# Optimization experiments

Hardware: AMD Instinct MI355X
Metric: run time of the kernel (lower is better)

## Reference

```python
import jax, jax.numpy as jnp
import numpy as np

SHIFT_SIZE = 5
PAD = 2  # shift_size // 2
EPS = 1e-5


def layernorm(x, g, b):
    m = x.mean(-1, keepdims=True)
    v = ((x - m) ** 2).mean(-1, keepdims=True)
    return (x - m) / jnp.sqrt(v + EPS) * g + b


def axial_shift(x, H, W, D, axis):
    # x: (B, N, C) -> torch-style shift along spatial `axis` of (B,C,H,W,D)
    B, N, C = x.shape
    xn = x.transpose(0, 2, 1).reshape(B, C, H, W, D)
    xn = jnp.pad(xn, ((0, 0), (0, 0), (PAD, PAD), (PAD, PAD), (PAD, PAD)))
    cs = -(-C // SHIFT_SIZE)  # torch.chunk uses ceil-sized chunks
    rolled = [
        jnp.roll(xn[:, i * cs:min((i + 1) * cs, C)], s, axis=axis)
        for i, s in enumerate(range(-PAD, PAD + 1))
    ]
    xc = jnp.concatenate(rolled, axis=1)
    xc = xc[:, :, PAD:PAD + H, PAD:PAD + W, PAD:PAD + D]
    return xc.reshape(B, C, H * W * D).transpose(0, 2, 1)


def dwconv3d(x, w, b, H, W, D):
    # x: (B,N,C), w: (C,1,3,3,3) depthwise
    B, N, C = x.shape
    v = x.transpose(0, 2, 1).reshape(B, C, H, W, D)
    y = jax.lax.conv_general_dilated(
        v, w, window_strides=(1, 1, 1), padding=[(1, 1)] * 3,
        dimension_numbers=('NCDHW', 'OIDHW', 'NCDHW'), feature_group_count=C)
    y = y + b[None, :, None, None, None]
    return y.reshape(B, C, N).transpose(0, 2, 1)


def setup_inputs() -> dict:
    key = jax.random.key(0)
    ks = jax.random.split(key, 12)
    C_in, C = 4, 128
    x = jax.random.normal(ks[0], (1, C_in, 96, 96, 96), dtype=jnp.float32)
    p = {
        'x': x,
        'proj_w': jax.random.normal(ks[1], (C, C_in, 3, 3, 3), jnp.float32) * 0.05,
        'proj_b': jnp.zeros((C,), jnp.float32),
        'g0': jnp.ones((C,), jnp.float32), 'b0': jnp.zeros((C,), jnp.float32),
        'g2': jnp.ones((C,), jnp.float32), 'b2': jnp.zeros((C,), jnp.float32),
        'fc1_w': jax.random.normal(ks[2], (C, C), jnp.float32) * 0.02,
        'fc1_b': jnp.zeros((C,), jnp.float32),
        'dw1_w': jax.random.normal(ks[3], (C, 1, 3, 3, 3), jnp.float32) * 0.1,
        'dw1_b': jnp.zeros((C,), jnp.float32),
        'fc2_w': jax.random.normal(ks[4], (C, C), jnp.float32) * 0.02,
        'fc2_b': jnp.zeros((C,), jnp.float32),
        'dw2_w': jax.random.normal(ks[5], (C, 1, 3, 3, 3), jnp.float32) * 0.1,
        'dw2_b': jnp.zeros((C,), jnp.float32),
        'fc3_w': jax.random.normal(ks[6], (C, C), jnp.float32) * 0.02,
        'fc3_b': jnp.zeros((C,), jnp.float32),
        'gn': jnp.ones((C,), jnp.float32), 'bn': jnp.zeros((C,), jnp.float32),
    }
    return p


def reference(x, proj_w, proj_b, g0, b0, g2, b2, fc1_w, fc1_b, dw1_w, dw1_b,
              fc2_w, fc2_b, dw2_w, dw2_b, fc3_w, fc3_b, gn, bn):
    B = x.shape[0]
    # OverlapPatchEmbed: Conv3d(k=3, s=2, p=1)
    v = jax.lax.conv_general_dilated(
        x, proj_w, window_strides=(2, 2, 2), padding=[(1, 1)] * 3,
        dimension_numbers=('NCDHW', 'OIDHW', 'NCDHW'))
    v = v + proj_b[None, :, None, None, None]
    _, C, H, W, D = v.shape
    t = v.reshape(B, C, H * W * D).transpose(0, 2, 1)  # (B,N,C)
    t = layernorm(t, g0, b0)

    # unext_shifted_Block (dropout/droppath in eval -> identity)
    h = layernorm(t, g2, b2)
    h = axial_shift(h, H, W, D, axis=2)
    h = h @ fc1_w.T + fc1_b
    h = dwconv3d(h, dw1_w, dw1_b, H, W, D)
    h = axial_shift(h, H, W, D, axis=3)
    h = h @ fc2_w.T + fc2_b
    h = dwconv3d(h, dw2_w, dw2_b, H, W, D)
    h = axial_shift(h, H, W, D, axis=4)
    h = h @ fc3_w.T + fc3_b
    h = jax.nn.gelu(h, approximate=False)
    t = t + h

    t = layernorm(t, gn, bn)
    out = t.reshape(B, H, W, D, C).transpose(0, 4, 1, 2, 3)
    return out
```

## Files before the change

kernel.cpp:

```cpp
#include <hip/hip_runtime.h>
#include <hip/hip_bf16.h>
#include <math.h>

#define NTOT 110592
#define SD 48
#define SWD 2304

typedef short s16x8 __attribute__((ext_vector_type(8)));
typedef unsigned short u16x8 __attribute__((ext_vector_type(8)));
typedef unsigned short u16x4 __attribute__((ext_vector_type(4)));
typedef float f32x4 __attribute__((ext_vector_type(4)));
typedef unsigned short u16;

__device__ __forceinline__ float bf2f(u16 u) {
    unsigned int x = ((unsigned int)u) << 16;
    float f; __builtin_memcpy(&f, &x, 4); return f;
}
__device__ __forceinline__ u16 f2bf(float f) {
    __hip_bfloat16 h = __float2bfloat16(f);
    u16 u; __builtin_memcpy(&u, &h, 2); return u;
}
__device__ __forceinline__ u16x8 zero8() {
    u16x8 z;
    #pragma unroll
    for (int j = 0; j < 8; ++j) z[j] = 0;
    return z;
}

__device__ __forceinline__ float gelu_f(float x) {
    float y = x * (0.7978845608f + 0.0356774081f * x * x);
    float e = exp2f(y * 2.885390082f);
    return x - x * __builtin_amdgcn_rcpf(e + 1.f);
}

__device__ __forceinline__ u16x8 ld_shift8(const u16* __restrict__ in, int n, int coord,
                                           int STR, int cbase) {
    int g = cbase / 26;
    int split = 26 * (g + 1) - cbase;
    int sh0 = g - 2;
    int cs0 = coord - sh0;
    u16x8 lo = zero8();
    if (cs0 >= 0 && cs0 < SD) lo = *(const u16x8*)&in[(size_t)(n - sh0 * STR) * 128 + cbase];
    if (split >= 8) return lo;
    u16x8 hi = zero8();
    int cs1 = cs0 - 1;
    if (cs1 >= 0 && cs1 < SD) hi = *(const u16x8*)&in[(size_t)(n - (sh0 + 1) * STR) * 128 + cbase];
    u16x8 r;
    #pragma unroll
    for (int j = 0; j < 8; ++j) r[j] = (j < split) ? lo[j] : hi[j];
    return r;
}

__device__ __forceinline__ int dec_tap(int tau) {
    int ti = (tau >= 18 ? 1 : 0) + (tau >= 9 ? 1 : 0);
    int rem = tau - ti * 9;
    int tj = (rem >= 6 ? 1 : 0) + (rem >= 3 ? 1 : 0);
    int tk = rem - tj * 3;
    return ti * 2080 + tj * 416 + tk * 4;
}

__global__ __launch_bounds__(256) void k_prep(
    const float* __restrict__ pw, const float* __restrict__ fc1w,
    const float* __restrict__ fc2w, const float* __restrict__ fc3w,
    const float* __restrict__ dw1w, const float* __restrict__ dw2w,
    u16* __restrict__ wfP, u16* __restrict__ wf1, u16* __restrict__ wf2,
    u16* __restrict__ wf3, float* __restrict__ dwT1, float* __restrict__ dwT2)
{
    int b = blockIdx.x;
    if (b < 32) {
        int which = b >> 3;
        const float* src = (which == 0) ? pw : (which == 1) ? fc1w : (which == 2) ? fc2w : fc3w;
        u16* dst = (which == 0) ? wfP : (which == 1) ? wf1 : (which == 2) ? wf2 : wf3;
        int idx = (b & 7) * 256 + threadIdx.x;
        int lane = idx & 63;
        int s = (idx >> 6) & 3;
        int t = idx >> 8;
        int co = t * 16 + (lane & 15);
        int kb = s * 32 + (lane >> 4) * 8;
        #pragma unroll
        for (int j = 0; j < 8; ++j) {
            int kk = kb + j;
            float v;
            if (which == 0) {
                int tau = kk >> 2, ci = kk & 3;
                v = (tau < 27) ? src[co * 108 + ci * 27 + tau] : 0.f;
            } else {
                v = src[co * 128 + kk];
            }
            dst[idx * 8 + j] = f2bf(v);
        }
    } else {
        int which = (b - 32) / 14;
        int bb = (b - 32) % 14;
        const float* src = which ? dw2w : dw1w;
        float* dst = which ? dwT2 : dwT1;
        int idx = bb * 256 + threadIdx.x;
        if (idx < 27 * 128) {
            int k = idx >> 7;
            int co = idx & 127;
            dst[idx] = src[co * 27 + k];
        }
    }
}

__global__ __launch_bounds__(384) void k_proj_ln(
    const float* __restrict__ x, const u16* __restrict__ wfrag, const float* __restrict__ pb,
    const float* __restrict__ g0, const float* __restrict__ b0,
    const float* __restrict__ g2, const float* __restrict__ b2,
    u16* __restrict__ t_out, u16* __restrict__ h_out)
{
    __shared__ __align__(16) u16 sm[15 * 104 * 4];
    __shared__ __align__(16) u16 wfl[16384];
    const int tid = threadIdx.x;
    const int blk = blockIdx.x;
    const int n0 = blk * 96;
    const int oi = blk / 24;
    const int oj0 = (blk % 24) * 2;

    for (int i = tid; i < 2048; i += 384)
        *(u16x8*)&wfl[i * 8] = *(const u16x8*)&wfrag[i * 8];

    for (int pos = tid; pos < 15 * 98; pos += 384) {
        int r = pos / 98;
        int p = pos - r * 98;
        int ti = r / 5, sl = r - ti * 5;
        int iig = 2 * oi + ti - 1;
        int ijg = 2 * oj0 + sl - 1;
        int ik = p - 1;
        bool okv = (iig >= 0) && (iig < 96) && (ijg >= 0) && (ijg < 96) && (ik >= 0) && (ik < 96);
        u16x4 v;
        #pragma unroll
        for (int ci = 0; ci < 4; ++ci)
            v[ci] = okv ? f2bf(x[(((size_t)ci * 96 + iig) * 96 + ijg) * 96 + ik]) : (u16)0;
        *(u16x4*)&sm[(r * 104 + p) * 4] = v;
    }
    __syncthreads();

    const int lane = tid & 63;
    const int wv = tid >> 6;
    const int rb = wv * 16;
    const int colb = lane & 15;
    const int q = lane >> 4;
    const int arow = rb + colb;
    const int ojloc = (arow >= 48) ? 1 : 0;
    const int okk = arow - ojloc * 48;
    const int P = ojloc * 832 + okk * 8;

    int S[4][2];
    #pragma unroll
    for (int s = 0; s < 4; ++s) {
        int t0 = s * 8 + 2 * q;
        S[s][0] = dec_tap(t0);
        S[s][1] = dec_tap(t0 + 1);
    }

    f32x4 acc[8];
    #pragma unroll
    for (int t = 0; t < 8; ++t) {
        float bb = pb[t * 16 + colb];
        acc[t][0] = bb; acc[t][1] = bb; acc[t][2] = bb; acc[t][3] = bb;
    }
    #pragma unroll
    for (int s = 0; s < 4; ++s) {
        u16x4 v0 = *(const u16x4*)&sm[S[s][0] + P];
        u16x4 v1 = *(const u16x4*)&sm[S[s][1] + P];
        if (s == 3) {
            bool z0 = (q >= 2), z1 = (q >= 1);
            #pragma unroll
            for (int e = 0; e < 4; ++e) {
                if (z0) v0[e] = 0;
                if (z1) v1[e] = 0;
            }
        }
        s16x8 a;
        a[0] = (short)v0[0]; a[1] = (short)v0[1]; a[2] = (short)v0[2]; a[3] = (short)v0[3];
        a[4] = (short)v1[0]; a[5] = (short)v1[1]; a[6] = (short)v1[2]; a[7] = (short)v1[3];
        s16x8 bf[8];
        #pragma unroll
        for (int t = 0; t < 8; ++t)
            bf[t] = *(const s16x8*)&wfl[((t * 4 + s) * 64 + lane) * 8];
        #pragma unroll
        for (int t = 0; t < 8; ++t)
            acc[t] = __builtin_amdgcn_mfma_f32_16x16x32_bf16(a, bf[t], acc[t], 0, 0, 0);
    }

    float s1[4] = {0.f,0.f,0.f,0.f}, s2[4] = {0.f,0.f,0.f,0.f};
    #pragma unroll
    for (int t = 0; t < 8; ++t)
        #pragma unroll
        for (int r4 = 0; r4 < 4; ++r4) {
            float v = acc[t][r4];
            s1[r4] += v; s2[r4] += v * v;
        }
    #pragma unroll
    for (int r4 = 0; r4 < 4; ++r4)
        #pragma unroll
        for (int m = 1; m < 16; m <<= 1) {
            s1[r4] += __shfl_xor(s1[r4], m);
            s2[r4] += __shfl_xor(s2[r4], m);
        }

    float g0v[8], b0v[8], g2v[8], b2v[8];
    #pragma unroll
    for (int t = 0; t < 8; ++t) {
        int c = t * 16 + colb;
        g0v[t] = g0[c]; b0v[t] = b0[c]; g2v[t] = g2[c]; b2v[t] = b2[c];
    }

    float tval[8][4];
    float u1[4] = {0.f,0.f,0.f,0.f}, u2[4] = {0.f,0.f,0.f,0.f};
    #pragma unroll
    for (int r4 = 0; r4 < 4; ++r4) {
        float mean = s1[r4] * (1.f / 128.f);
        float var  = fmaxf(s2[r4] * (1.f / 128.f) - mean * mean, 0.f);
        float rstd = rsqrtf(var + 1e-5f);
        #pragma unroll
        for (int t = 0; t < 8; ++t) {
            float tv = (acc[t][r4] - mean) * rstd * g0v[t] + b0v[t];
            tval[t][r4] = tv;
            u1[r4] += tv; u2[r4] += tv * tv;
        }
    }
    #pragma unroll
    for (int r4 = 0; r4 < 4; ++r4) {
        #pragma unroll
        for (int m = 1; m < 16; m <<= 1) {
            u1[r4] += __shfl_xor(u1[r4], m);
            u2[r4] += __shfl_xor(u2[r4], m);
        }
    }

    #pragma unroll
    for (int r4 = 0; r4 < 4; ++r4) {
        float mean2 = u1[r4] * (1.f / 128.f);
        float var2  = fmaxf(u2[r4] * (1.f / 128.f) - mean2 * mean2, 0.f);
        float rstd2 = rsqrtf(var2 + 1e-5f);
        int row = rb + q * 4 + r4;
        size_t base = (size_t)(n0 + row) * 128;
        #pragma unroll
        for (int t = 0; t < 8; ++t) {
            int col = t * 16 + colb;
            float tv = tval[t][r4];
            t_out[base + col] = f2bf(tv);
            float hv = (tv - mean2) * rstd2 * g2v[t] + b2v[t];
            h_out[base + col] = f2bf(hv);
        }
    }
}

template <int AXIS>
__global__ __launch_bounds__(256) void k_shift_mm(
    const u16* __restrict__ in, const u16* __restrict__ wfrag, const float* __restrict__ bias,
    u16* __restrict__ out)
{
    __shared__ __align__(16) u16 wfl[16384];
    const int tid = threadIdx.x;
    const int n0 = blockIdx.x * 64;
    const int lane = tid & 63;
    const int wv = tid >> 6;
    const int colb = lane & 15;
    const int q = lane >> 4;

    for (int i = tid; i < 2048; i += 256)
        *(u16x8*)&wfl[i * 8] = *(const u16x8*)&wfrag[i * 8];

    const int arow = wv * 16 + colb;
    const int n = n0 + arow;
    const int STR = (AXIS == 0) ? SWD : (AXIS == 1) ? SD : 1;
    const int coord = (AXIS == 0) ? n / SWD : (AXIS == 1) ? (n / SD) % SD : n % SD;

    f32x4 acc[8];
    #pragma unroll
    for (int t = 0; t < 8; ++t) {
        float bb = bias[t * 16 + colb];
        acc[t][0] = bb; acc[t][1] = bb; acc[t][2] = bb; acc[t][3] = bb;
    }
    __syncthreads();
    #pragma unroll
    for (int s = 0; s < 4; ++s) {
        u16x8 av = ld_shift8(in, n, coord, STR, s * 32 + q * 8);
        s16x8 a = *(s16x8*)&av;
        s16x8 bf[8];
        #pragma unroll
        for (int t = 0; t < 8; ++t)
            bf[t] = *(const s16x8*)&wfl[((t * 4 + s) * 64 + lane) * 8];
        #pragma unroll
        for (int t = 0; t < 8; ++t)
            acc[t] = __builtin_amdgcn_mfma_f32_16x16x32_bf16(a, bf[t], acc[t], 0, 0, 0);
    }
    #pragma unroll
    for (int r4 = 0; r4 < 4; ++r4) {
        int row = wv * 16 + q * 4 + r4;
        size_t base = (size_t)(n0 + row) * 128;
        #pragma unroll
        for (int t = 0; t < 8; ++t)
            out[base + t * 16 + colb] = f2bf(acc[t][r4]);
    }
}

__global__ __launch_bounds__(256, 4) void k_dw(
    const u16* __restrict__ in, const float* __restrict__ wt, const float* __restrict__ b,
    u16* __restrict__ out)
{
    __shared__ __align__(16) float wtl[27 * 128];
    const int tid = threadIdx.x;
    const int cg = tid & 15;
    const int kq = tid >> 4;
    const int k0 = kq * 3;
    const int bid = blockIdx.x;
    const int ij = (bid & 7) * 288 + (bid >> 3);
    const int i = ij / SD;
    const int j = ij - i * SD;
    const int c = cg * 8;

    for (int t = tid; t < 864; t += 256)
        ((float4*)wtl)[t] = ((const float4*)wt)[t];

    const int kclamp0 = (k0 - 1 < 0) ? 0 : (k0 - 1);
    const int kclamp4 = (k0 + 3 > SD - 1) ? (SD - 1) : (k0 + 3);
    const bool k0bad = (k0 - 1 < 0);
    const bool k4bad = (k0 + 3 > SD - 1);

    float acc[3][8];
    {
        float4 ba = *(const float4*)&b[c];
        float4 bb = *(const float4*)&b[c + 4];
        #pragma unroll
        for (int t = 0; t < 3; ++t) {
            acc[t][0] = ba.x; acc[t][1] = ba.y; acc[t][2] = ba.z; acc[t][3] = ba.w;
            acc[t][4] = bb.x; acc[t][5] = bb.y; acc[t][6] = bb.z; acc[t][7] = bb.w;
        }
    }

    bool okt[9];
    const u16* baseptr[9];
    #pragma unroll
    for (int t9 = 0; t9 < 9; ++t9) {
        int di = t9 / 3 - 1, dj = t9 % 3 - 1;
        int ii = i + di, jj = j + dj;
        okt[t9] = ((unsigned)ii < SD) && ((unsigned)jj < SD);
        int iic = (ii < 0) ? 0 : (ii > SD - 1 ? SD - 1 : ii);
        int jjc = (jj < 0) ? 0 : (jj > SD - 1 ? SD - 1 : jj);
        baseptr[t9] = &in[(size_t)((iic * SD + jjc) * SD) * 128 + c];
    }

    u16x8 win[2][5];
    {
        const u16* base = baseptr[0];
        win[0][0] = *(const u16x8*)(base + (size_t)kclamp0 * 128);
        win[0][1] = *(const u16x8*)(base + (size_t)(k0    ) * 128);
        win[0][2] = *(const u16x8*)(base + (size_t)(k0 + 1) * 128);
        win[0][3] = *(const u16x8*)(base + (size_t)(k0 + 2) * 128);
        win[0][4] = *(const u16x8*)(base + (size_t)kclamp4 * 128);
    }
    __syncthreads();

    #pragma unroll
    for (int t9 = 0; t9 < 9; ++t9) {
        const int cur = t9 & 1;
        if (t9 < 8) {
            const u16* base = baseptr[t9 + 1];
            win[cur ^ 1][0] = *(const u16x8*)(base + (size_t)kclamp0 * 128);
            win[cur ^ 1][1] = *(const u16x8*)(base + (size_t)(k0    ) * 128);
            win[cur ^ 1][2] = *(const u16x8*)(base + (size_t)(k0 + 1) * 128);
            win[cur ^ 1][3] = *(const u16x8*)(base + (size_t)(k0 + 2) * 128);
            win[cur ^ 1][4] = *(const u16x8*)(base + (size_t)kclamp4 * 128);
        }
        if (okt[t9]) {
            const int tap0 = t9 * 3;
            float wv[3][8];
            #pragma unroll
            for (int dk = 0; dk < 3; ++dk) {
                float4 wa = *(const float4*)&wtl[(tap0 + dk) * 128 + c];
                float4 wb = *(const float4*)&wtl[(tap0 + dk) * 128 + c + 4];
                wv[dk][0] = wa.x; wv[dk][1] = wa.y; wv[dk][2] = wa.z; wv[dk][3] = wa.w;
                wv[dk][4] = wb.x; wv[dk][5] = wb.y; wv[dk][6] = wb.z; wv[dk][7] = wb.w;
            }
            #pragma unroll
            for (int s = 0; s < 5; ++s) {
                bool bad = (s == 0 && k0bad) || (s == 4 && k4bad);
                float vs[8];
                #pragma unroll
                for (int m = 0; m < 8; ++m)
                    vs[m] = bad ? 0.f : bf2f(win[cur][s][m]);
                #pragma unroll
                for (int t = 0; t < 3; ++t) {
                    int dk = s - t;
                    if (dk >= 0 && dk < 3) {
                        #pragma unroll
                        for (int m = 0; m < 8; ++m)
                            acc[t][m] = fmaf(wv[dk][m], vs[m], acc[t][m]);
                    }
                }
            }
        }
    }
    #pragma unroll
    for (int t = 0; t < 3; ++t) {
        u16x8 o;
        #pragma unroll
        for (int m = 0; m < 8; ++m) o[m] = f2bf(acc[t][m]);
        *(u16x8*)&out[(size_t)((i * SD + j) * SD + k0 + t) * 128 + c] = o;
    }
}

__global__ __launch_bounds__(256) void k_final(
    const u16* __restrict__ in, const u16* __restrict__ wfrag, const float* __restrict__ bias,
    const u16* __restrict__ tin, const float* __restrict__ gn, const float* __restrict__ bn,
    float* __restrict__ out)
{
    __shared__ u16 T[64 * 136];
    __shared__ __align__(16) u16 wfl[16384];
    const int tid = threadIdx.x;
    const int n0 = blockIdx.x * 64;
    const int lane = tid & 63;
    const int wv = tid >> 6;
    const int colb = lane & 15;
    const int q = lane >> 4;

    for (int i = tid; i < 2048; i += 256)
        *(u16x8*)&wfl[i * 8] = *(const u16x8*)&wfrag[i * 8];

    for (int i = tid; i < 1024; i += 256) {
        int row = i >> 4;
        int c8 = (i & 15) * 8;
        *(u16x8*)&T[row * 136 + c8] = *(const u16x8*)&tin[(size_t)(n0 + row) * 128 + c8];
    }

    const int nn = wv * 16 + colb;
    const int n = n0 + nn;
    const int coord = n % SD;

    f32x4 acc[8];
    #pragma unroll
    for (int ta = 0; ta < 8; ++ta)
        #pragma unroll
        for (int r4 = 0; r4 < 4; ++r4)
            acc[ta][r4] = bias[ta * 16 + q * 4 + r4];
    __syncthreads();

    #pragma unroll
    for (int s = 0; s < 4; ++s) {
        u16x8 bv = ld_shift8(in, n, coord, 1, s * 32 + q * 8);
        s16x8 b = *(s16x8*)&bv;
        s16x8 af[8];
        #pragma unroll
        for (int ta = 0; ta < 8; ++ta)
            af[ta] = *(const s16x8*)&wfl[((ta * 4 + s) * 64 + lane) * 8];
        #pragma unroll
        for (int ta = 0; ta < 8; ++ta)
            acc[ta] = __builtin_amdgcn_mfma_f32_16x16x32_bf16(af[ta], b, acc[ta], 0, 0, 0);
    }

    float val[8][4];
    float s1 = 0.f, s2 = 0.f;
    #pragma unroll
    for (int ta = 0; ta < 8; ++ta)
        #pragma unroll
        for (int r4 = 0; r4 < 4; ++r4) {
            int co = ta * 16 + q * 4 + r4;
            float v = gelu_f(acc[ta][r4]) + bf2f(T[nn * 136 + co]);
            val[ta][r4] = v;
            s1 += v; s2 += v * v;
        }
    s1 += __shfl_xor(s1, 16); s2 += __shfl_xor(s2, 16);
    s1 += __shfl_xor(s1, 32); s2 += __shfl_xor(s2, 32);
    float mean = s1 * (1.f / 128.f);
    float var  = fmaxf(s2 * (1.f / 128.f) - mean * mean, 0.f);
    float rstd = rsqrtf(var + 1e-5f);

    #pragma unroll
    for (int ta = 0; ta < 8; ++ta)
        #pragma unroll
        for (int r4 = 0; r4 < 4; ++r4) {
            int co = ta * 16 + q * 4 + r4;
            float o = (val[ta][r4] - mean) * rstd * gn[co] + bn[co];
            out[(size_t)co * NTOT + n] = o;
        }
}

extern "C" void kernel_launch(void* const* d_in, const int* in_sizes, int n_in,
                              void* d_out, int out_size, void* d_ws, size_t ws_size,
                              hipStream_t stream)
{
    const float* x    = (const float*)d_in[0];
    const float* pw   = (const float*)d_in[1];
    const float* pb   = (const float*)d_in[2];
    const float* g0   = (const float*)d_in[3];
    const float* b0   = (const float*)d_in[4];
    const float* g2   = (const float*)d_in[5];
    const float* b2   = (const float*)d_in[6];
    const float* fc1w = (const float*)d_in[7];
    const float* fc1b = (const float*)d_in[8];
    const float* dw1w = (const float*)d_in[9];
    const float* dw1b = (const float*)d_in[10];
    const float* fc2w = (const float*)d_in[11];
    const float* fc2b = (const float*)d_in[12];
    const float* dw2w = (const float*)d_in[13];
    const float* dw2b = (const float*)d_in[14];
    const float* fc3w = (const float*)d_in[15];
    const float* fc3b = (const float*)d_in[16];
    const float* gn   = (const float*)d_in[17];
    const float* bn   = (const float*)d_in[18];
    float* out = (float*)d_out;

    u16* tbuf = (u16*)d_ws;
    u16* h1   = tbuf + (size_t)NTOT * 128;
    u16* h2   = h1 + (size_t)NTOT * 128;
    u16* wfP  = h2 + (size_t)NTOT * 128;
    u16* wf1  = wfP + 16384;
    u16* wf2  = wf1 + 16384;
    u16* wf3  = wf2 + 16384;
    float* dwT1 = (float*)(wf3 + 16384);
    float* dwT2 = dwT1 + 27 * 128;

    k_prep<<<60, 256, 0, stream>>>(pw, fc1w, fc2w, fc3w, dw1w, dw2w,
                                   wfP, wf1, wf2, wf3, dwT1, dwT2);

    k_proj_ln<<<NTOT / 96, 384, 0, stream>>>(x, wfP, pb, g0, b0, g2, b2, tbuf, h1);
    k_shift_mm<0><<<NTOT / 64, 256, 0, stream>>>(h1, wf1, fc1b, h2);
    k_dw<<<SWD, 256, 0, stream>>>(h2, dwT1, dw1b, h1);
    k_shift_mm<1><<<NTOT / 64, 256, 0, stream>>>(h1, wf2, fc2b, h2);
    k_dw<<<SWD, 256, 0, stream>>>(h2, dwT2, dw2b, h1);
    k_final<<<NTOT / 64, 256, 0, stream>>>(h1, wf3, fc3b, tbuf, gn, bn, out);
}
```

Before: 159.1 us.

## Load weight fragments straight into registers and vectorize proj input staging

Each lane now loads its own MFMA weight fragments from global memory into registers instead of the whole block copying all weights into shared memory and then re-reading them. This removes the shared-memory staging, the LDS traffic and the __syncthreads in the shift-matmul and final kernels. The final kernel also reads its residual t values directly into registers rather than through an LDS tile. The projection kernel loads x with float4 vector reads and zeroes only the halo, relying on the fact that only the leading borders can fall outside the input. The cost is much higher register pressure, since 32 fragments are held per lane, which may lower occupancy, and redundant global loads of the weights that hit in L2.

```diff
diff --git a/kernel.cpp b/kernel.cpp
--- a/kernel.cpp
+++ b/kernel.cpp
@@ -110,33 +110,52 @@
     u16* __restrict__ t_out, u16* __restrict__ h_out)
 {
     __shared__ __align__(16) u16 sm[15 * 104 * 4];
-    __shared__ __align__(16) u16 wfl[16384];
     const int tid = threadIdx.x;
     const int blk = blockIdx.x;
     const int n0 = blk * 96;
     const int oi = blk / 24;
     const int oj0 = (blk % 24) * 2;
 
-    for (int i = tid; i < 2048; i += 384)
-        *(u16x8*)&wfl[i * 8] = *(const u16x8*)&wfrag[i * 8];
-
-    for (int pos = tid; pos < 15 * 98; pos += 384) {
-        int r = pos / 98;
-        int p = pos - r * 98;
+    const int lane = tid & 63;
+
+    s16x8 wreg[8][4];
+    #pragma unroll
+    for (int t = 0; t < 8; ++t)
+        #pragma unroll
+        for (int s = 0; s < 4; ++s)
+            wreg[t][s] = *(const s16x8*)&wfrag[((t * 4 + s) * 64 + lane) * 8];
+
+    if (tid < 15) {
+        u16x4 z; z[0] = 0; z[1] = 0; z[2] = 0; z[3] = 0;
+        *(u16x4*)&sm[(tid * 104 + 0) * 4] = z;
+    }
+    if (tid < 360) {
+        int r = tid / 24;
+        int a = tid - r * 24;
         int ti = r / 5, sl = r - ti * 5;
         int iig = 2 * oi + ti - 1;
         int ijg = 2 * oj0 + sl - 1;
-        int ik = p - 1;
-        bool okv = (iig >= 0) && (iig < 96) && (ijg >= 0) && (ijg < 96) && (ik >= 0) && (ik < 96);
-        u16x4 v;
-        #pragma unroll
-        for (int ci = 0; ci < 4; ++ci)
-            v[ci] = okv ? f2bf(x[(((size_t)ci * 96 + iig) * 96 + ijg) * 96 + ik]) : (u16)0;
-        *(u16x4*)&sm[(r * 104 + p) * 4] = v;
+        float4 v[4];
+        if (iig >= 0 && ijg >= 0) {
+            #pragma unroll
+            for (int ci = 0; ci < 4; ++ci)
+                v[ci] = *(const float4*)&x[(((size_t)ci * 96 + iig) * 96 + ijg) * 96 + 4 * a];
+        } else {
+            #pragma unroll
+            for (int ci = 0; ci < 4; ++ci) v[ci] = make_float4(0.f, 0.f, 0.f, 0.f);
+        }
+        #pragma unroll
+        for (int j = 0; j < 4; ++j) {
+            u16x4 w;
+            w[0] = f2bf(((const float*)&v[0])[j]);
+            w[1] = f2bf(((const float*)&v[1])[j]);
+            w[2] = f2bf(((const float*)&v[2])[j]);
+            w[3] = f2bf(((const float*)&v[3])[j]);
+            *(u16x4*)&sm[(r * 104 + 4 * a + 1 + j) * 4] = w;
+        }
     }
     __syncthreads();
 
-    const int lane = tid & 63;
     const int wv = tid >> 6;
     const int rb = wv * 16;
     const int colb = lane & 15;
@@ -175,13 +194,9 @@
         s16x8 a;
         a[0] = (short)v0[0]; a[1] = (short)v0[1]; a[2] = (short)v0[2]; a[3] = (short)v0[3];
         a[4] = (short)v1[0]; a[5] = (short)v1[1]; a[6] = (short)v1[2]; a[7] = (short)v1[3];
-        s16x8 bf[8];
         #pragma unroll
         for (int t = 0; t < 8; ++t)
-            bf[t] = *(const s16x8*)&wfl[((t * 4 + s) * 64 + lane) * 8];
-        #pragma unroll
-        for (int t = 0; t < 8; ++t)
-            acc[t] = __builtin_amdgcn_mfma_f32_16x16x32_bf16(a, bf[t], acc[t], 0, 0, 0);
+            acc[t] = __builtin_amdgcn_mfma_f32_16x16x32_bf16(a, wreg[t][s], acc[t], 0, 0, 0);
     }
 
     float s1[4] = {0.f,0.f,0.f,0.f}, s2[4] = {0.f,0.f,0.f,0.f};
@@ -253,7 +268,6 @@
     const u16* __restrict__ in, const u16* __restrict__ wfrag, const float* __restrict__ bias,
     u16* __restrict__ out)
 {
-    __shared__ __align__(16) u16 wfl[16384];
     const int tid = threadIdx.x;
     const int n0 = blockIdx.x * 64;
     const int lane = tid & 63;
@@ -261,8 +275,12 @@
     const int colb = lane & 15;
     const int q = lane >> 4;
 
-    for (int i = tid; i < 2048; i += 256)
-        *(u16x8*)&wfl[i * 8] = *(const u16x8*)&wfrag[i * 8];
+    s16x8 wreg[8][4];
+    #pragma unroll
+    for (int t = 0; t < 8; ++t)
+        #pragma unroll
+        for (int s = 0; s < 4; ++s)
+            wreg[t][s] = *(const s16x8*)&wfrag[((t * 4 + s) * 64 + lane) * 8];
 
     const int arow = wv * 16 + colb;
     const int n = n0 + arow;
@@ -275,18 +293,13 @@
         float bb = bias[t * 16 + colb];
         acc[t][0] = bb; acc[t][1] = bb; acc[t][2] = bb; acc[t][3] = bb;
     }
-    __syncthreads();
     #pragma unroll
     for (int s = 0; s < 4; ++s) {
         u16x8 av = ld_shift8(in, n, coord, STR, s * 32 + q * 8);
         s16x8 a = *(s16x8*)&av;
-        s16x8 bf[8];
         #pragma unroll
         for (int t = 0; t < 8; ++t)
-            bf[t] = *(const s16x8*)&wfl[((t * 4 + s) * 64 + lane) * 8];
-        #pragma unroll
-        for (int t = 0; t < 8; ++t)
-            acc[t] = __builtin_amdgcn_mfma_f32_16x16x32_bf16(a, bf[t], acc[t], 0, 0, 0);
+            acc[t] = __builtin_amdgcn_mfma_f32_16x16x32_bf16(a, wreg[t][s], acc[t], 0, 0, 0);
     }
     #pragma unroll
     for (int r4 = 0; r4 < 4; ++r4) {
@@ -409,8 +422,6 @@
     const u16* __restrict__ tin, const float* __restrict__ gn, const float* __restrict__ bn,
     float* __restrict__ out)
 {
-    __shared__ u16 T[64 * 136];
-    __shared__ __align__(16) u16 wfl[16384];
     const int tid = threadIdx.x;
     const int n0 = blockIdx.x * 64;
     const int lane = tid & 63;
@@ -418,38 +429,36 @@
     const int colb = lane & 15;
     const int q = lane >> 4;
 
-    for (int i = tid; i < 2048; i += 256)
-        *(u16x8*)&wfl[i * 8] = *(const u16x8*)&wfrag[i * 8];
-
-    for (int i = tid; i < 1024; i += 256) {
-        int row = i >> 4;
-        int c8 = (i & 15) * 8;
-        *(u16x8*)&T[row * 136 + c8] = *(const u16x8*)&tin[(size_t)(n0 + row) * 128 + c8];
-    }
-
     const int nn = wv * 16 + colb;
     const int n = n0 + nn;
     const int coord = n % SD;
 
+    u16x4 tq[8];
+    #pragma unroll
+    for (int ta = 0; ta < 8; ++ta)
+        tq[ta] = *(const u16x4*)&tin[(size_t)n * 128 + ta * 16 + q * 4];
+
+    s16x8 wreg[8][4];
+    #pragma unroll
+    for (int ta = 0; ta < 8; ++ta)
+        #pragma unroll
+        for (int s = 0; s < 4; ++s)
+            wreg[ta][s] = *(const s16x8*)&wfrag[((ta * 4 + s) * 64 + lane) * 8];
+
     f32x4 acc[8];
     #pragma unroll
     for (int ta = 0; ta < 8; ++ta)
         #pragma unroll
         for (int r4 = 0; r4 < 4; ++r4)
             acc[ta][r4] = bias[ta * 16 + q * 4 + r4];
-    __syncthreads();
 
     #pragma unroll
     for (int s = 0; s < 4; ++s) {
         u16x8 bv = ld_shift8(in, n, coord, 1, s * 32 + q * 8);
         s16x8 b = *(s16x8*)&bv;
-        s16x8 af[8];
         #pragma unroll
         for (int ta = 0; ta < 8; ++ta)
-            af[ta] = *(const s16x8*)&wfl[((ta * 4 + s) * 64 + lane) * 8];
-        #pragma unroll
-        for (int ta = 0; ta < 8; ++ta)
-            acc[ta] = __builtin_amdgcn_mfma_f32_16x16x32_bf16(af[ta], b, acc[ta], 0, 0, 0);
+            acc[ta] = __builtin_amdgcn_mfma_f32_16x16x32_bf16(wreg[ta][s], b, acc[ta], 0, 0, 0);
     }
 
     float val[8][4];
@@ -458,8 +467,7 @@
     for (int ta = 0; ta < 8; ++ta)
         #pragma unroll
         for (int r4 = 0; r4 < 4; ++r4) {
-            int co = ta * 16 + q * 4 + r4;
-            float v = gelu_f(acc[ta][r4]) + bf2f(T[nn * 136 + co]);
+            float v = gelu_f(acc[ta][r4]) + bf2f(tq[ta][r4]);
             val[ta][r4] = v;
             s1 += v; s2 += v * v;
         }
```

New measurement: 164.8 us. 3.6% more time.

## Gather proj conv inputs directly from global and stage final output transpose in LDS

Applied to the files above, without the earlier changes.

The patch-embed kernel drops its shared-memory input tile and instead has each lane gather its 3x3x3x4 stride-2 taps straight from global memory, with 64-row blocks of 256 threads. The final kernel now writes its normalized outputs into an LDS buffer that aliases the weight area, then emits channel-major rows as coalesced float4 stores instead of scattered scalar stores. The first change removes the LDS staging and its barrier but issues strided, uncoalesced global loads that depend on cache hits. The second adds two barriers and reuses LDS for the transpose.

```diff
diff --git a/kernel.cpp b/kernel.cpp
--- a/kernel.cpp
+++ b/kernel.cpp
@@ -49,14 +49,6 @@
     #pragma unroll
     for (int j = 0; j < 8; ++j) r[j] = (j < split) ? lo[j] : hi[j];
     return r;
-}
-
-__device__ __forceinline__ int dec_tap(int tau) {
-    int ti = (tau >= 18 ? 1 : 0) + (tau >= 9 ? 1 : 0);
-    int rem = tau - ti * 9;
-    int tj = (rem >= 6 ? 1 : 0) + (rem >= 3 ? 1 : 0);
-    int tk = rem - tj * 3;
-    return ti * 2080 + tj * 416 + tk * 4;
 }
 
 __global__ __launch_bounds__(256) void k_prep(
@@ -103,56 +95,30 @@
     }
 }
 
-__global__ __launch_bounds__(384) void k_proj_ln(
+__global__ __launch_bounds__(256) void k_proj_ln(
     const float* __restrict__ x, const u16* __restrict__ wfrag, const float* __restrict__ pb,
     const float* __restrict__ g0, const float* __restrict__ b0,
     const float* __restrict__ g2, const float* __restrict__ b2,
     u16* __restrict__ t_out, u16* __restrict__ h_out)
 {
-    __shared__ __align__(16) u16 sm[15 * 104 * 4];
     __shared__ __align__(16) u16 wfl[16384];
     const int tid = threadIdx.x;
-    const int blk = blockIdx.x;
-    const int n0 = blk * 96;
-    const int oi = blk / 24;
-    const int oj0 = (blk % 24) * 2;
-
-    for (int i = tid; i < 2048; i += 384)
-        *(u16x8*)&wfl[i * 8] = *(const u16x8*)&wfrag[i * 8];
-
-    for (int pos = tid; pos < 15 * 98; pos += 384) {
-        int r = pos / 98;
-        int p = pos - r * 98;
-        int ti = r / 5, sl = r - ti * 5;
-        int iig = 2 * oi + ti - 1;
-        int ijg = 2 * oj0 + sl - 1;
-        int ik = p - 1;
-        bool okv = (iig >= 0) && (iig < 96) && (ijg >= 0) && (ijg < 96) && (ik >= 0) && (ik < 96);
-        u16x4 v;
-        #pragma unroll
-        for (int ci = 0; ci < 4; ++ci)
-            v[ci] = okv ? f2bf(x[(((size_t)ci * 96 + iig) * 96 + ijg) * 96 + ik]) : (u16)0;
-        *(u16x4*)&sm[(r * 104 + p) * 4] = v;
-    }
-    __syncthreads();
-
+    const int n0 = blockIdx.x * 64;
     const int lane = tid & 63;
     const int wv = tid >> 6;
-    const int rb = wv * 16;
     const int colb = lane & 15;
     const int q = lane >> 4;
-    const int arow = rb + colb;
-    const int ojloc = (arow >= 48) ? 1 : 0;
-    const int okk = arow - ojloc * 48;
-    const int P = ojloc * 832 + okk * 8;
-
-    int S[4][2];
-    #pragma unroll
-    for (int s = 0; s < 4; ++s) {
-        int t0 = s * 8 + 2 * q;
-        S[s][0] = dec_tap(t0);
-        S[s][1] = dec_tap(t0 + 1);
-    }
+
+    for (int i = tid; i < 2048; i += 256)
+        *(u16x8*)&wfl[i * 8] = *(const u16x8*)&wfrag[i * 8];
+
+    const int arow = wv * 16 + colb;
+    const int n = n0 + arow;
+    const int oi = n / SWD;
+    const int rem = n - oi * SWD;
+    const int oj = rem / SD;
+    const int ok = rem - oj * SD;
+    const int ii0 = 2 * oi - 1, ij0 = 2 * oj - 1, ik0 = 2 * ok - 1;
 
     f32x4 acc[8];
     #pragma unroll
@@ -160,21 +126,33 @@
         float bb = pb[t * 16 + colb];
         acc[t][0] = bb; acc[t][1] = bb; acc[t][2] = bb; acc[t][3] = bb;
     }
+    __syncthreads();
+
     #pragma unroll
     for (int s = 0; s < 4; ++s) {
-        u16x4 v0 = *(const u16x4*)&sm[S[s][0] + P];
-        u16x4 v1 = *(const u16x4*)&sm[S[s][1] + P];
-        if (s == 3) {
-            bool z0 = (q >= 2), z1 = (q >= 1);
-            #pragma unroll
-            for (int e = 0; e < 4; ++e) {
-                if (z0) v0[e] = 0;
-                if (z1) v1[e] = 0;
+        s16x8 a;
+        #pragma unroll
+        for (int d = 0; d < 2; ++d) {
+            int tq = 2 * q + d;
+            int tau = s * 8 + tq;
+            u16 v4[4] = {0, 0, 0, 0};
+            bool valid = (s < 3) || (tq < 3);
+            if (valid) {
+                int ti = (tau >= 18 ? 1 : 0) + (tau >= 9 ? 1 : 0);
+                int r2 = tau - ti * 9;
+                int tj = (r2 >= 6 ? 1 : 0) + (r2 >= 3 ? 1 : 0);
+                int tk = r2 - tj * 3;
+                int ii = ii0 + ti, ij = ij0 + tj, ik = ik0 + tk;
+                if (ii >= 0 && ij >= 0 && ik >= 0) {
+                    size_t off = ((size_t)ii * 96 + ij) * 96 + ik;
+                    #pragma unroll
+                    for (int ci = 0; ci < 4; ++ci)
+                        v4[ci] = f2bf(x[(size_t)ci * 884736 + off]);
+                }
             }
-        }
-        s16x8 a;
-        a[0] = (short)v0[0]; a[1] = (short)v0[1]; a[2] = (short)v0[2]; a[3] = (short)v0[3];
-        a[4] = (short)v1[0]; a[5] = (short)v1[1]; a[6] = (short)v1[2]; a[7] = (short)v1[3];
+            a[4 * d + 0] = (short)v4[0]; a[4 * d + 1] = (short)v4[1];
+            a[4 * d + 2] = (short)v4[2]; a[4 * d + 3] = (short)v4[3];
+        }
         s16x8 bf[8];
         #pragma unroll
         for (int t = 0; t < 8; ++t)
@@ -235,7 +213,7 @@
         float mean2 = u1[r4] * (1.f / 128.f);
         float var2  = fmaxf(u2[r4] * (1.f / 128.f) - mean2 * mean2, 0.f);
         float rstd2 = rsqrtf(var2 + 1e-5f);
-        int row = rb + q * 4 + r4;
+        int row = wv * 16 + q * 4 + r4;
         size_t base = (size_t)(n0 + row) * 128;
         #pragma unroll
         for (int t = 0; t < 8; ++t) {
@@ -409,8 +387,10 @@
     const u16* __restrict__ tin, const float* __restrict__ gn, const float* __restrict__ bn,
     float* __restrict__ out)
 {
-    __shared__ u16 T[64 * 136];
-    __shared__ __align__(16) u16 wfl[16384];
+    __shared__ __align__(16) unsigned char smem[50176];
+    u16* wfl = (u16*)smem;
+    u16* T = (u16*)(smem + 32768);
+    float* Osm = (float*)smem;
     const int tid = threadIdx.x;
     const int n0 = blockIdx.x * 64;
     const int lane = tid & 63;
@@ -420,7 +400,6 @@
 
     for (int i = tid; i < 2048; i += 256)
         *(u16x8*)&wfl[i * 8] = *(const u16x8*)&wfrag[i * 8];
-
     for (int i = tid; i < 1024; i += 256) {
         int row = i >> 4;
         int c8 = (i & 15) * 8;
@@ -452,7 +431,6 @@
             acc[ta] = __builtin_amdgcn_mfma_f32_16x16x32_bf16(af[ta], b, acc[ta], 0, 0, 0);
     }
 
-    float val[8][4];
     float s1 = 0.f, s2 = 0.f;
     #pragma unroll
     for (int ta = 0; ta < 8; ++ta)
@@ -460,7 +438,7 @@
         for (int r4 = 0; r4 < 4; ++r4) {
             int co = ta * 16 + q * 4 + r4;
             float v = gelu_f(acc[ta][r4]) + bf2f(T[nn * 136 + co]);
-            val[ta][r4] = v;
+            acc[ta][r4] = v;
             s1 += v; s2 += v * v;
         }
     s1 += __shfl_xor(s1, 16); s2 += __shfl_xor(s2, 16);
@@ -469,14 +447,26 @@
     float var  = fmaxf(s2 * (1.f / 128.f) - mean * mean, 0.f);
     float rstd = rsqrtf(var + 1e-5f);
 
+    __syncthreads();
+
     #pragma unroll
     for (int ta = 0; ta < 8; ++ta)
         #pragma unroll
         for (int r4 = 0; r4 < 4; ++r4) {
             int co = ta * 16 + q * 4 + r4;
-            float o = (val[ta][r4] - mean) * rstd * gn[co] + bn[co];
-            out[(size_t)co * NTOT + n] = o;
-        }
+            float o = (acc[ta][r4] - mean) * rstd * gn[co] + bn[co];
+            Osm[co * 68 + nn] = o;
+        }
+    __syncthreads();
+
+    #pragma unroll
+    for (int it = 0; it < 8; ++it) {
+        int idx = it * 256 + tid;
+        int row = idx >> 4;
+        int c4 = idx & 15;
+        f32x4 v = *(const f32x4*)&Osm[row * 68 + c4 * 4];
+        *(f32x4*)&out[(size_t)row * NTOT + n0 + c4 * 4] = v;
+    }
 }
 
 extern "C" void kernel_launch(void* const* d_in, const int* in_sizes, int n_in,
@@ -517,7 +507,7 @@
     k_prep<<<60, 256, 0, stream>>>(pw, fc1w, fc2w, fc3w, dw1w, dw2w,
                                    wfP, wf1, wf2, wf3, dwT1, dwT2);
 
-    k_proj_ln<<<NTOT / 96, 384, 0, stream>>>(x, wfP, pb, g0, b0, g2, b2, tbuf, h1);
+    k_proj_ln<<<NTOT / 64, 256, 0, stream>>>(x, wfP, pb, g0, b0, g2, b2, tbuf, h1);
     k_shift_mm<0><<<NTOT / 64, 256, 0, stream>>>(h1, wf1, fc1b, h2);
     k_dw<<<SWD, 256, 0, stream>>>(h2, dwT1, dw1b, h1);
     k_shift_mm<1><<<NTOT / 64, 256, 0, stream>>>(h1, wf2, fc2b, h2);
```

Result: faster. 149.2 us (-6.2%).
